# Kernel tuning notes

Measured on AMD Instinct MI355X. Metric: run time of the kernel, lower is better.

The kernel has to match this reference:

```python
import jax, jax.numpy as jnp
import numpy as np
from jax import lax

WIN_H, WIN_W = 4, 7            # window_size
GRID_OFF = (0.0, 40.0)         # grid_offsets
SPATIAL_SCALE = 1.0 / 0.4      # 1 / featmap_stride
BN_EPS = 1e-3


def setup_inputs() -> dict:
    key = jax.random.key(0)
    ks = jax.random.split(key, 4)
    B, Cin, H, W, N, P = 4, 256, 200, 176, 2048, 28
    x = jax.random.normal(ks[0], (B, Cin, H, W), jnp.float32)
    # realistic KITTI-style 3D boxes: x,y,z,w,l,h,r
    u = jax.random.uniform(ks[1], (B, N, 7), jnp.float32)
    lo = jnp.array([0.0, -40.0, -3.0, 1.4, 3.2, 1.4, -np.pi], jnp.float32)
    hi = jnp.array([70.4, 40.0, 1.0, 2.0, 4.6, 1.8, np.pi], jnp.float32)
    boxes = lo + u * (hi - lo)
    conv1_w = jax.random.normal(ks[2], (P, Cin, 3, 3), jnp.float32) * 0.02
    conv2_w = jax.random.normal(ks[3], (P, P, 1, 1), jnp.float32) * 0.1
    bn_gamma = jnp.ones((P,), jnp.float32)
    bn_beta = jnp.zeros((P,), jnp.float32)
    bn_mean = jnp.zeros((P,), jnp.float32)
    bn_var = jnp.ones((P,), jnp.float32)
    return dict(x=x, boxes=boxes, conv1_w=conv1_w, bn_gamma=bn_gamma,
                bn_beta=bn_beta, bn_mean=bn_mean, bn_var=bn_var, conv2_w=conv2_w)


def _bilinear_zeros(img, xs, ys):
    # img: (H, W); xs, ys: (N,) pixel coords. Zeros padding, align_corners=True
    # semantics (the torch code normalizes by (W-1)/(H-1), i.e. pixel coords).
    H, W = img.shape
    x0 = jnp.floor(xs)
    y0 = jnp.floor(ys)
    x1 = x0 + 1.0
    y1 = y0 + 1.0

    def gather(yi, xi):
        valid = (xi >= 0) & (xi <= W - 1) & (yi >= 0) & (yi <= H - 1)
        xi_c = jnp.clip(xi, 0, W - 1).astype(jnp.int32)
        yi_c = jnp.clip(yi, 0, H - 1).astype(jnp.int32)
        return jnp.where(valid, img[yi_c, xi_c], 0.0)

    Ia = gather(y0, x0)
    Ib = gather(y1, x0)
    Ic = gather(y0, x1)
    Id = gather(y1, x1)
    wa = (x1 - xs) * (y1 - ys)
    wb = (x1 - xs) * (ys - y0)
    wc = (xs - x0) * (y1 - ys)
    wd = (xs - x0) * (ys - y0)
    return wa * Ia + wb * Ib + wc * Ic + wd * Id


def reference(x, boxes, conv1_w, bn_gamma, bn_beta, bn_mean, bn_var, conv2_w):
    dn = ('NCHW', 'OIHW', 'NCHW')
    feat = lax.conv_general_dilated(x, conv1_w, (1, 1), 'SAME', dimension_numbers=dn)
    inv_std = bn_gamma / jnp.sqrt(bn_var + BN_EPS)
    scale = inv_std[None, :, None, None]
    shift = (bn_beta - bn_mean * inv_std)[None, :, None, None]
    feat = jax.nn.relu(feat * scale + shift)
    feat = lax.conv_general_dilated(feat, conv2_w, (1, 1), 'SAME', dimension_numbers=dn)  # (B,P,H,W)

    # rotated sampling grid: boxes[:, :, [0,1,3,4,6]] = (x, y, w, l, r)
    xg, yg, wg, lg, rg = (boxes[..., i] for i in (0, 1, 3, 4, 6))  # each (B,N)
    cosT = jnp.cos(rg)[..., None, None]
    sinT = jnp.sin(rg)[..., None, None]
    lin_x = jnp.linspace(-0.5, 0.5, WIN_H)[:, None]     # (4,1)
    lin_y = jnp.linspace(-0.5, 0.5, WIN_W)[None, :]     # (1,7)
    xx = lin_x * wg[..., None, None]                    # (B,N,4,1)
    yy = lin_y * lg[..., None, None]                    # (B,N,1,7)
    gx = xx * cosT + yy * sinT + xg[..., None, None]    # (B,N,4,7)
    gy = yy * cosT - xx * sinT + yg[..., None, None]    # (B,N,4,7)
    gx = (gx + GRID_OFF[0]) * SPATIAL_SCALE
    gy = (gy + GRID_OFF[1]) * SPATIAL_SCALE
    B, N = xg.shape
    P = WIN_H * WIN_W
    gx = gx.transpose(0, 2, 3, 1).reshape(B, P, N)      # (B,28,N), part = window cell
    gy = gy.transpose(0, 2, 3, 1).reshape(B, P, N)

    # each part-channel p samples its own window cell -> (B,P,N)
    sample = jax.vmap(jax.vmap(_bilinear_zeros))
    out = sample(feat, gx, gy)                          # (B,P,N)
    scores = out.mean(axis=1)                           # (B,N) mean over parts
    return scores.reshape(-1)                           # torch.cat over batch
```

## Files before the change

### kernel.cpp

```cpp
#include <hip/hip_runtime.h>
#include <hip/hip_bf16.h>


#define WDIM 176
#define HDIM 200
#define HWDIM 35200
#define CIN 256
#define PDIM 28
#define NBOX 2048

typedef __attribute__((ext_vector_type(8))) short bf16x8;
typedef __attribute__((ext_vector_type(4))) float floatx4;
typedef __attribute__((ext_vector_type(16))) float floatx16;

__device__ __forceinline__ unsigned short f2bf(float f) {
    unsigned int u; __builtin_memcpy(&u, &f, 4);
    unsigned int r = u + 0x7FFFu + ((u >> 16) & 1u);
    return (unsigned short)(r >> 16);
}

__global__ __launch_bounds__(256) void transpose_kernel(const float* __restrict__ x,
                                                        unsigned short* __restrict__ xT2) {
    __shared__ unsigned short st[64][72];
    int b = blockIdx.z, c0 = blockIdx.y * 64, px0 = blockIdx.x * 64;
    int t = threadIdx.x;

    int c_l = t >> 2, pq = t & 3;
    const float* sp = x + (long)(b * CIN + c0 + c_l) * HWDIM + px0 + pq * 16;
    float4 v0 = ((const float4*)sp)[0], v1 = ((const float4*)sp)[1];
    float4 v2 = ((const float4*)sp)[2], v3 = ((const float4*)sp)[3];
    int pr = pq * 16;
    st[pr +  0][c_l] = f2bf(v0.x); st[pr +  1][c_l] = f2bf(v0.y);
    st[pr +  2][c_l] = f2bf(v0.z); st[pr +  3][c_l] = f2bf(v0.w);
    st[pr +  4][c_l] = f2bf(v1.x); st[pr +  5][c_l] = f2bf(v1.y);
    st[pr +  6][c_l] = f2bf(v1.z); st[pr +  7][c_l] = f2bf(v1.w);
    st[pr +  8][c_l] = f2bf(v2.x); st[pr +  9][c_l] = f2bf(v2.y);
    st[pr + 10][c_l] = f2bf(v2.z); st[pr + 11][c_l] = f2bf(v2.w);
    st[pr + 12][c_l] = f2bf(v3.x); st[pr + 13][c_l] = f2bf(v3.y);
    st[pr + 14][c_l] = f2bf(v3.z); st[pr + 15][c_l] = f2bf(v3.w);
    __syncthreads();

    int w = t >> 6, l = t & 63;
    int ks = (c0 >> 4) + w;
    long pbase = ((long)(b * 16 + ks) * HWDIM + px0) * 16;
#pragma unroll
    for (int i = 0; i < 2; i++) {
        int px_l = i * 32 + (l >> 1);
        int hc = l & 1;
        bf16x8 frag = *(const bf16x8*)&st[px_l][w * 16 + hc * 8];
        *(bf16x8*)(xT2 + pbase + px_l * 16 + hc * 8) = frag;
    }
}

__global__ void prep_kernel(const float* __restrict__ w1,
                            const float* __restrict__ g, const float* __restrict__ bt,
                            const float* __restrict__ mn, const float* __restrict__ vr,
                            unsigned short* __restrict__ BwT2,
                            float* __restrict__ scale, float* __restrict__ shift) {
    int idx = blockIdx.x * 256 + threadIdx.x;
    if (idx < 9 * 16 * 64 * 8) {
        int f = idx >> 9;
        int tap = f >> 4, ks = f & 15;
        int l = (idx >> 3) & 63;
        int e = idx & 7;
        int n = l & 31, kh = l >> 5;
        int c = ks * 16 + kh * 8 + e;
        BwT2[idx] = (n < PDIM) ? f2bf(w1[n * 2304 + c * 9 + tap]) : (unsigned short)0;
    } else if (idx < 73728 + 32) {
        int p = idx - 73728;
        if (p < PDIM) {
            float inv = g[p] / sqrtf(vr[p] + 1e-3f);
            scale[p] = inv;
            shift[p] = bt[p] - mn[p] * inv;
        } else { scale[p] = 0.f; shift[p] = 0.f; }
    }
}

__global__ __launch_bounds__(64) void conv1_kernel(const unsigned short* __restrict__ xT2,
                                                   const unsigned short* __restrict__ BwT2,
                                                   const float* __restrict__ scale,
                                                   const float* __restrict__ shift,
                                                   const float* __restrict__ w2,
                                                   float* __restrict__ feat2) {
    __shared__ float t2f[32 * 36];

    int wg = blockIdx.y * 1200 + blockIdx.x;
    int nl = (wg & 7) * 600 + (wg >> 3);
    int b = nl / 1200;
    int rem = nl - b * 1200;
    int y = rem / 6, win = rem - (rem / 6) * 6;
    int pxbase = win * 32;

    int lane = threadIdx.x;
    int r32 = lane & 31, khalf = lane >> 5;

    bool rowok[3];
#pragma unroll
    for (int rr = 0; rr < 3; rr++) rowok[rr] = (y + rr - 1 >= 0) && (y + rr - 1 < HDIM);
    bool edge = (win == 0) || (win == 5);

    bool xval[3];
    int  voff[3];
#pragma unroll
    for (int d = 0; d < 3; d++) {
        int xp = pxbase + r32 + d - 1;
        xval[d] = (xp >= 0) && (xp < WDIM);
        int xc = xp < 0 ? 0 : (xp > WDIM - 1 ? WDIM - 1 : xp);
        voff[d] = xc * 32 + khalf * 16;
    }

    const char* abase[3];
#pragma unroll
    for (int rr = 0; rr < 3; rr++) {
        int yc = y + rr - 1;
        yc = yc < 0 ? 0 : (yc > HDIM - 1 ? HDIM - 1 : yc);
        abase[rr] = (const char*)xT2 + ((long)b * 16 * HWDIM + (long)yc * WDIM) * 32;
    }
    const long KS = (long)HWDIM * 32;
    const char* bb = (const char*)BwT2 + lane * 16;

    bf16x8 aq[2][9];
#pragma unroll
    for (int t = 0; t < 9; t++)
        aq[0][t] = *(const bf16x8*)(abase[t / 3] + voff[t % 3]);

    floatx16 acc = {};

#pragma unroll
    for (int s = 0; s < 16; s++) {
        const int cur = s & 1, nxt = cur ^ 1;
        bf16x8 bq[9];
#pragma unroll
        for (int t = 0; t < 9; t++)
            bq[t] = *(const bf16x8*)(bb + t * 16384 + s * 1024);
        if (s < 15) {
#pragma unroll
            for (int t = 0; t < 9; t++)
                aq[nxt][t] = *(const bf16x8*)(abase[t / 3] + KS * (s + 1) + voff[t % 3]);
            __builtin_amdgcn_sched_barrier(0);
            asm volatile("s_waitcnt vmcnt(18)" ::: "memory");
        } else {
            __builtin_amdgcn_sched_barrier(0);
            asm volatile("s_waitcnt vmcnt(9)" ::: "memory");
        }
        __builtin_amdgcn_sched_barrier(0);
        if (!edge) {
#pragma unroll
            for (int t = 0; t < 9; t++) {
                if (!rowok[t / 3]) continue;
                acc = __builtin_amdgcn_mfma_f32_32x32x16_bf16(aq[cur][t], bq[t], acc, 0, 0, 0);
            }
        } else {
#pragma unroll
            for (int t = 0; t < 9; t++) {
                if (!rowok[t / 3]) continue;
                bf16x8 af = aq[cur][t];
                if (!xval[t % 3]) af = (bf16x8)0;
                acc = __builtin_amdgcn_mfma_f32_32x32x16_bf16(af, bq[t], acc, 0, 0, 0);
            }
        }
    }

    {
        float sc = scale[r32], sh2 = shift[r32];
#pragma unroll
        for (int i = 0; i < 16; i++) {
            int prow = (i & 3) + 8 * (i >> 2) + 4 * khalf;
            float v = fmaf(acc[i], sc, sh2);
            t2f[prow * 36 + r32] = v > 0.f ? v : 0.f;
        }
    }
    long rowpix = (long)b * HWDIM + (long)y * WDIM;
    int n_l = r32;
    float4 w2r[7];
#pragma unroll
    for (int jj = 0; jj < 7; jj++) {
        if (n_l < PDIM) w2r[jj] = ((const float4*)(w2 + n_l * PDIM))[jj];
        else            w2r[jj] = make_float4(0.f, 0.f, 0.f, 0.f);
    }
#pragma unroll
    for (int i = 0; i < 16; i++) {
        int pxl = khalf * 16 + i;
        float s = 0.f;
#pragma unroll
        for (int jj = 0; jj < 7; jj++) {
            float4 a = *(const float4*)&t2f[pxl * 36 + jj * 4];
            s = fmaf(a.x, w2r[jj].x, s); s = fmaf(a.y, w2r[jj].y, s);
            s = fmaf(a.z, w2r[jj].z, s); s = fmaf(a.w, w2r[jj].w, s);
        }
        int px = pxbase + pxl;
        if (n_l < PDIM && px < WDIM) feat2[(rowpix + px) * PDIM + n_l] = s;
    }
}

__global__ __launch_bounds__(256) void sample_kernel(const float* __restrict__ boxes,
                                                     const float* __restrict__ feat2,
                                                     float* __restrict__ out) {
    int gid = blockIdx.x * 256 + threadIdx.x;
    int box = gid >> 5;
    int pl = gid & 31;
    int b = box >> 11;
    float val = 0.f;
    if (pl < PDIM) {
        long bb = (long)box * 7;
        float xg = boxes[bb + 0], yg = boxes[bb + 1];
        float wg = boxes[bb + 3], lg = boxes[bb + 4];
        float rg = boxes[bb + 6];
        float ct = cosf(rg), st = sinf(rg);
        const float lxv[4] = {-0.5f, -0.16666667f, 0.16666667f, 0.5f};
        const float lyv[7] = {-0.5f, -0.33333334f, -0.16666667f, 0.f,
                               0.16666667f, 0.33333334f, 0.5f};
        int h = pl / 7, ww = pl - (pl / 7) * 7;
        float xx = lxv[h] * wg;
        float yy = lyv[ww] * lg;
        float gx = (xx * ct + yy * st + xg) * 2.5f;
        float gy = (yy * ct - xx * st + yg + 40.f) * 2.5f;
        float x0 = floorf(gx), y0 = floorf(gy);
        float fx = gx - x0, fy = gy - y0;
        int xi = (int)x0, yi = (int)y0;
        const float* base = feat2 + (long)b * HWDIM * PDIM + pl;
        float Ia = 0.f, Ib = 0.f, Ic = 0.f, Id = 0.f;
        if (yi >= 0 && yi < HDIM) {
            long r0 = (long)yi * WDIM;
            if (xi >= 0 && xi < WDIM)         Ia = base[(r0 + xi) * PDIM];
            if (xi + 1 >= 0 && xi + 1 < WDIM) Ic = base[(r0 + xi + 1) * PDIM];
        }
        if (yi + 1 >= 0 && yi + 1 < HDIM) {
            long r1 = (long)(yi + 1) * WDIM;
            if (xi >= 0 && xi < WDIM)         Ib = base[(r1 + xi) * PDIM];
            if (xi + 1 >= 0 && xi + 1 < WDIM) Id = base[(r1 + xi + 1) * PDIM];
        }
        val = (1.f - fx) * (1.f - fy) * Ia + (1.f - fx) * fy * Ib
            + fx * (1.f - fy) * Ic + fx * fy * Id;
    }
#pragma unroll
    for (int m = 16; m >= 1; m >>= 1) val += __shfl_xor(val, m, 64);
    if ((threadIdx.x & 31) == 0) {
        out[box] = val * (1.f / 28.f);
    }
}

extern "C" void kernel_launch(void* const* d_in, const int* in_sizes, int n_in,
                              void* d_out, int out_size, void* d_ws, size_t ws_size,
                              hipStream_t stream) {
    const float* x     = (const float*)d_in[0];
    const float* boxes = (const float*)d_in[1];
    const float* w1    = (const float*)d_in[2];
    const float* g     = (const float*)d_in[3];
    const float* bt    = (const float*)d_in[4];
    const float* mn    = (const float*)d_in[5];
    const float* vr    = (const float*)d_in[6];
    const float* w2    = (const float*)d_in[7];
    float* out = (float*)d_out;

    char* ws = (char*)d_ws;
    unsigned short* xT2  = (unsigned short*)ws;
    float* feat2         = (float*)(ws + 72089600);
    unsigned short* BwT2 = (unsigned short*)(ws + 90112000);
    float* scale         = (float*)(ws + 90259456);
    float* shift         = (float*)(ws + 90259584);

    transpose_kernel<<<dim3(550, 4, 4), 256, 0, stream>>>(x, xT2);
    prep_kernel<<<289, 256, 0, stream>>>(w1, g, bt, mn, vr, BwT2, scale, shift);
    conv1_kernel<<<dim3(1200, 4), 64, 0, stream>>>(xT2, BwT2, scale, shift, w2, feat2);
    sample_kernel<<<1024, 256, 0, stream>>>(boxes, feat2, out);
}
```

Baseline: 284.9 us.

## Share conv weight tiles across six waves via async global-to-LDS staging

The conv1 kernel changes from one 64-thread wave per 32-pixel window to a 384-thread block covering a whole image row with six waves. The weight (B) fragments are no longer loaded by every wave from global memory. The block loads them once with global_load_lds async copies into a 6-slot LDS ring and reads them from LDS, using manual vmcnt waits and barriers to pipeline this. The aim is to cut redundant weight traffic from global memory, at the cost of block-level barriers, more LDS use and tighter manual wait counting.

```diff
diff --git a/kernel.cpp b/kernel.cpp
--- a/kernel.cpp
+++ b/kernel.cpp
@@ -17,6 +17,12 @@
     unsigned int u; __builtin_memcpy(&u, &f, 4);
     unsigned int r = u + 0x7FFFu + ((u >> 16) & 1u);
     return (unsigned short)(r >> 16);
+}
+
+__device__ __forceinline__ void async_copy16(const void* g, void* l) {
+    __builtin_amdgcn_global_load_lds(
+        (const __attribute__((address_space(1))) void*)g,
+        (__attribute__((address_space(3))) void*)l, 16, 0, 0);
 }
 
 __global__ __launch_bounds__(256) void transpose_kernel(const float* __restrict__ x,
@@ -76,28 +82,27 @@
     }
 }
 
-__global__ __launch_bounds__(64) void conv1_kernel(const unsigned short* __restrict__ xT2,
-                                                   const unsigned short* __restrict__ BwT2,
-                                                   const float* __restrict__ scale,
-                                                   const float* __restrict__ shift,
-                                                   const float* __restrict__ w2,
-                                                   float* __restrict__ feat2) {
-    __shared__ float t2f[32 * 36];
-
-    int wg = blockIdx.y * 1200 + blockIdx.x;
-    int nl = (wg & 7) * 600 + (wg >> 3);
-    int b = nl / 1200;
-    int rem = nl - b * 1200;
-    int y = rem / 6, win = rem - (rem / 6) * 6;
-    int pxbase = win * 32;
-
-    int lane = threadIdx.x;
+__global__ __launch_bounds__(384) void conv1_kernel(const unsigned short* __restrict__ xT2,
+                                                    const unsigned short* __restrict__ BwT2,
+                                                    const float* __restrict__ scale,
+                                                    const float* __restrict__ shift,
+                                                    const float* __restrict__ w2,
+                                                    float* __restrict__ feat2) {
+    __shared__ unsigned short Bs[6 * 9 * 512];
+
+    int wg = blockIdx.y * 200 + blockIdx.x;
+    int nl = (wg & 7) * 100 + (wg >> 3);
+    int b = nl / 200, y = nl % 200;
+
+    int lane = threadIdx.x & 63, w = threadIdx.x >> 6;
     int r32 = lane & 31, khalf = lane >> 5;
+    int lane16 = lane * 16;
+    int pxbase = w * 32;
 
     bool rowok[3];
 #pragma unroll
     for (int rr = 0; rr < 3; rr++) rowok[rr] = (y + rr - 1 >= 0) && (y + rr - 1 < HDIM);
-    bool edge = (win == 0) || (win == 5);
+    bool edge = (w == 0) || (w == 5);
 
     bool xval[3];
     int  voff[3];
@@ -117,50 +122,91 @@
         abase[rr] = (const char*)xT2 + ((long)b * 16 * HWDIM + (long)yc * WDIM) * 32;
     }
     const long KS = (long)HWDIM * 32;
-    const char* bb = (const char*)BwT2 + lane * 16;
-
+    const char* bwb = (const char*)BwT2;
+
+#define STAGE_PAIR(s2) {                                                      \
+        _Pragma("unroll")                                                     \
+        for (int k = 0; k < 3; k++) {                                         \
+            int F = 3 * w + k;                                                \
+            int stp = (s2) + (F >= 9 ? 1 : 0);                                \
+            int tap = F >= 9 ? F - 9 : F;                                     \
+            async_copy16(bwb + tap * 16384 + stp * 1024 + lane16,             \
+                         (char*)Bs + (stp % 6) * 9216 + tap * 1024);          \
+        }                                                                     \
+    }
+
+    STAGE_PAIR(0)
+    STAGE_PAIR(2)
     bf16x8 aq[2][9];
 #pragma unroll
     for (int t = 0; t < 9; t++)
         aq[0][t] = *(const bf16x8*)(abase[t / 3] + voff[t % 3]);
+    __builtin_amdgcn_sched_barrier(0);
+    asm volatile("s_waitcnt vmcnt(9)" ::: "memory");
+    __builtin_amdgcn_sched_barrier(0);
+    asm volatile("s_barrier" ::: "memory");
 
     floatx16 acc = {};
 
-#pragma unroll
-    for (int s = 0; s < 16; s++) {
-        const int cur = s & 1, nxt = cur ^ 1;
-        bf16x8 bq[9];
-#pragma unroll
-        for (int t = 0; t < 9; t++)
-            bq[t] = *(const bf16x8*)(bb + t * 16384 + s * 1024);
-        if (s < 15) {
+#define DO_MFMA(AQ)                                                           \
+        if (!edge) {                                                          \
+            _Pragma("unroll")                                                 \
+            for (int t = 0; t < 9; t++) {                                     \
+                if (!rowok[t / 3]) continue;                                  \
+                acc = __builtin_amdgcn_mfma_f32_32x32x16_bf16(AQ[t], bq[t], acc, 0, 0, 0); \
+            }                                                                 \
+        } else {                                                              \
+            _Pragma("unroll")                                                 \
+            for (int t = 0; t < 9; t++) {                                     \
+                if (!rowok[t / 3]) continue;                                  \
+                bf16x8 af = AQ[t];                                            \
+                if (!xval[t % 3]) af = (bf16x8)0;                             \
+                acc = __builtin_amdgcn_mfma_f32_32x32x16_bf16(af, bq[t], acc, 0, 0, 0); \
+            }                                                                 \
+        }
+
+#pragma unroll
+    for (int S = 0; S < 8; S++) {
+        const int s0 = 2 * S, s1 = 2 * S + 1;
+        {
+            if (S <= 5) STAGE_PAIR(2 * S + 4)
 #pragma unroll
             for (int t = 0; t < 9; t++)
-                aq[nxt][t] = *(const bf16x8*)(abase[t / 3] + KS * (s + 1) + voff[t % 3]);
+                aq[1][t] = *(const bf16x8*)(abase[t / 3] + KS * s1 + voff[t % 3]);
+            bf16x8 bq[9];
+#pragma unroll
+            for (int t = 0; t < 9; t++)
+                bq[t] = *(const bf16x8*)((const char*)Bs + (s0 % 6) * 9216 + t * 1024 + lane16);
             __builtin_amdgcn_sched_barrier(0);
-            asm volatile("s_waitcnt vmcnt(18)" ::: "memory");
-        } else {
+            if (S <= 5) { asm volatile("s_waitcnt vmcnt(12)" ::: "memory"); }
+            else        { asm volatile("s_waitcnt vmcnt(9)"  ::: "memory"); }
             __builtin_amdgcn_sched_barrier(0);
-            asm volatile("s_waitcnt vmcnt(9)" ::: "memory");
-        }
-        __builtin_amdgcn_sched_barrier(0);
-        if (!edge) {
-#pragma unroll
-            for (int t = 0; t < 9; t++) {
-                if (!rowok[t / 3]) continue;
-                acc = __builtin_amdgcn_mfma_f32_32x32x16_bf16(aq[cur][t], bq[t], acc, 0, 0, 0);
+            DO_MFMA(aq[0])
+        }
+        {
+            if (S <= 6) {
+#pragma unroll
+                for (int t = 0; t < 9; t++)
+                    aq[0][t] = *(const bf16x8*)(abase[t / 3] + KS * (s1 + 1) + voff[t % 3]);
             }
-        } else {
-#pragma unroll
-            for (int t = 0; t < 9; t++) {
-                if (!rowok[t / 3]) continue;
-                bf16x8 af = aq[cur][t];
-                if (!xval[t % 3]) af = (bf16x8)0;
-                acc = __builtin_amdgcn_mfma_f32_32x32x16_bf16(af, bq[t], acc, 0, 0, 0);
-            }
-        }
-    }
-
+            bf16x8 bq[9];
+#pragma unroll
+            for (int t = 0; t < 9; t++)
+                bq[t] = *(const bf16x8*)((const char*)Bs + (s1 % 6) * 9216 + t * 1024 + lane16);
+            __builtin_amdgcn_sched_barrier(0);
+            if (S <= 6) { asm volatile("s_waitcnt vmcnt(9)" ::: "memory"); }
+            else        { asm volatile("s_waitcnt vmcnt(0)" ::: "memory"); }
+            __builtin_amdgcn_sched_barrier(0);
+            DO_MFMA(aq[1])
+            if (S <= 5) { asm volatile("s_barrier" ::: "memory"); }
+        }
+    }
+#undef DO_MFMA
+#undef STAGE_PAIR
+
+    __syncthreads();
+
+    float* t2f = (float*)Bs + w * (32 * 36);
     {
         float sc = scale[r32], sh2 = shift[r32];
 #pragma unroll
@@ -262,6 +308,6 @@
 
     transpose_kernel<<<dim3(550, 4, 4), 256, 0, stream>>>(x, xT2);
     prep_kernel<<<289, 256, 0, stream>>>(w1, g, bt, mn, vr, BwT2, scale, shift);
-    conv1_kernel<<<dim3(1200, 4), 64, 0, stream>>>(xT2, BwT2, scale, shift, w2, feat2);
+    conv1_kernel<<<dim3(200, 4), 384, 0, stream>>>(xT2, BwT2, scale, shift, w2, feat2);
     sample_kernel<<<1024, 256, 0, stream>>>(boxes, feat2, out);
 }
```

Result: slower. 301.6 us (+5.9%).

## Compute two 32-pixel MFMA tiles per conv workgroup to reuse weight fragments

Applied to the files above, without the earlier changes.

Each conv1 workgroup now covers 64 pixels of a row, as two 32-pixel M tiles with separate accumulators, instead of 32 pixels. The grid is halved to match. Each loaded weight fragment feeds two MFMA tiles, which halves weight loads per output pixel. Activation prefetch for the second tile is interleaved after the first tile's MFMAs, and the wait counts are adjusted to match. The cost is more VGPRs for the doubled activation buffers and fewer workgroups, which can lower occupancy and latency hiding.

```diff
diff --git a/kernel.cpp b/kernel.cpp
--- a/kernel.cpp
+++ b/kernel.cpp
@@ -84,12 +84,12 @@
                                                    float* __restrict__ feat2) {
     __shared__ float t2f[32 * 36];
 
-    int wg = blockIdx.y * 1200 + blockIdx.x;
-    int nl = (wg & 7) * 600 + (wg >> 3);
-    int b = nl / 1200;
-    int rem = nl - b * 1200;
-    int y = rem / 6, win = rem - (rem / 6) * 6;
-    int pxbase = win * 32;
+    int wg = blockIdx.y * 600 + blockIdx.x;
+    int nl = (wg & 7) * 300 + (wg >> 3);
+    int b = nl / 600;
+    int rem = nl - b * 600;
+    int y = rem / 3, win = rem - (rem / 3) * 3;
+    int pxbase = win * 64;
 
     int lane = threadIdx.x;
     int r32 = lane & 31, khalf = lane >> 5;
@@ -97,16 +97,19 @@
     bool rowok[3];
 #pragma unroll
     for (int rr = 0; rr < 3; rr++) rowok[rr] = (y + rr - 1 >= 0) && (y + rr - 1 < HDIM);
-    bool edge = (win == 0) || (win == 5);
-
-    bool xval[3];
-    int  voff[3];
-#pragma unroll
-    for (int d = 0; d < 3; d++) {
-        int xp = pxbase + r32 + d - 1;
-        xval[d] = (xp >= 0) && (xp < WDIM);
-        int xc = xp < 0 ? 0 : (xp > WDIM - 1 ? WDIM - 1 : xp);
-        voff[d] = xc * 32 + khalf * 16;
+    bool edge0 = (win == 0), edge1 = (win == 2);
+
+    bool xval[2][3];
+    int  voff[2][3];
+#pragma unroll
+    for (int mt = 0; mt < 2; mt++) {
+#pragma unroll
+        for (int d = 0; d < 3; d++) {
+            int xp = pxbase + mt * 32 + r32 + d - 1;
+            xval[mt][d] = (xp >= 0) && (xp < WDIM);
+            int xc = xp < 0 ? 0 : (xp > WDIM - 1 ? WDIM - 1 : xp);
+            voff[mt][d] = xc * 32 + khalf * 16;
+        }
     }
 
     const char* abase[3];
@@ -119,12 +122,12 @@
     const long KS = (long)HWDIM * 32;
     const char* bb = (const char*)BwT2 + lane * 16;
 
-    bf16x8 aq[2][9];
-#pragma unroll
-    for (int t = 0; t < 9; t++)
-        aq[0][t] = *(const bf16x8*)(abase[t / 3] + voff[t % 3]);
-
-    floatx16 acc = {};
+    bf16x8 aq[2][18];
+#pragma unroll
+    for (int f = 0; f < 18; f++)
+        aq[0][f] = *(const bf16x8*)(abase[(f % 9) / 3] + voff[f / 9][f % 3]);
+
+    floatx16 acc0 = {}, acc1 = {};
 
 #pragma unroll
     for (int s = 0; s < 16; s++) {
@@ -136,60 +139,87 @@
         if (s < 15) {
 #pragma unroll
             for (int t = 0; t < 9; t++)
-                aq[nxt][t] = *(const bf16x8*)(abase[t / 3] + KS * (s + 1) + voff[t % 3]);
+                aq[nxt][t] = *(const bf16x8*)(abase[t / 3] + KS * (s + 1) + voff[0][t % 3]);
             __builtin_amdgcn_sched_barrier(0);
-            asm volatile("s_waitcnt vmcnt(18)" ::: "memory");
+            asm volatile("s_waitcnt vmcnt(9)" ::: "memory");
         } else {
             __builtin_amdgcn_sched_barrier(0);
-            asm volatile("s_waitcnt vmcnt(9)" ::: "memory");
+            asm volatile("s_waitcnt vmcnt(0)" ::: "memory");
         }
         __builtin_amdgcn_sched_barrier(0);
-        if (!edge) {
-#pragma unroll
-            for (int t = 0; t < 9; t++) {
-                if (!rowok[t / 3]) continue;
-                acc = __builtin_amdgcn_mfma_f32_32x32x16_bf16(aq[cur][t], bq[t], acc, 0, 0, 0);
+
+        if (!edge0) {
+#pragma unroll
+            for (int t = 0; t < 9; t++) {
+                if (!rowok[t / 3]) continue;
+                acc0 = __builtin_amdgcn_mfma_f32_32x32x16_bf16(aq[cur][t], bq[t], acc0, 0, 0, 0);
             }
         } else {
 #pragma unroll
             for (int t = 0; t < 9; t++) {
                 if (!rowok[t / 3]) continue;
                 bf16x8 af = aq[cur][t];
-                if (!xval[t % 3]) af = (bf16x8)0;
-                acc = __builtin_amdgcn_mfma_f32_32x32x16_bf16(af, bq[t], acc, 0, 0, 0);
-            }
-        }
-    }
-
-    {
-        float sc = scale[r32], sh2 = shift[r32];
+                if (!xval[0][t % 3]) af = (bf16x8)0;
+                acc0 = __builtin_amdgcn_mfma_f32_32x32x16_bf16(af, bq[t], acc0, 0, 0, 0);
+            }
+        }
+
+        if (s < 15) {
+#pragma unroll
+            for (int t = 0; t < 9; t++)
+                aq[nxt][9 + t] = *(const bf16x8*)(abase[t / 3] + KS * (s + 1) + voff[1][t % 3]);
+        }
+        __builtin_amdgcn_sched_barrier(0);
+
+        if (!edge1) {
+#pragma unroll
+            for (int t = 0; t < 9; t++) {
+                if (!rowok[t / 3]) continue;
+                acc1 = __builtin_amdgcn_mfma_f32_32x32x16_bf16(aq[cur][9 + t], bq[t], acc1, 0, 0, 0);
+            }
+        } else {
+#pragma unroll
+            for (int t = 0; t < 9; t++) {
+                if (!rowok[t / 3]) continue;
+                bf16x8 af = aq[cur][9 + t];
+                if (!xval[1][t % 3]) af = (bf16x8)0;
+                acc1 = __builtin_amdgcn_mfma_f32_32x32x16_bf16(af, bq[t], acc1, 0, 0, 0);
+            }
+        }
+    }
+
+    long rowpix = (long)b * HWDIM + (long)y * WDIM;
+    int n_l = r32;
+    float4 w2r[7];
+#pragma unroll
+    for (int jj = 0; jj < 7; jj++) {
+        if (n_l < PDIM) w2r[jj] = ((const float4*)(w2 + n_l * PDIM))[jj];
+        else            w2r[jj] = make_float4(0.f, 0.f, 0.f, 0.f);
+    }
+    float sc = scale[r32], sh2 = shift[r32];
+
+#pragma unroll
+    for (int mt = 0; mt < 2; mt++) {
+        const floatx16& acc = mt ? acc1 : acc0;
 #pragma unroll
         for (int i = 0; i < 16; i++) {
             int prow = (i & 3) + 8 * (i >> 2) + 4 * khalf;
             float v = fmaf(acc[i], sc, sh2);
             t2f[prow * 36 + r32] = v > 0.f ? v : 0.f;
         }
-    }
-    long rowpix = (long)b * HWDIM + (long)y * WDIM;
-    int n_l = r32;
-    float4 w2r[7];
-#pragma unroll
-    for (int jj = 0; jj < 7; jj++) {
-        if (n_l < PDIM) w2r[jj] = ((const float4*)(w2 + n_l * PDIM))[jj];
-        else            w2r[jj] = make_float4(0.f, 0.f, 0.f, 0.f);
-    }
-#pragma unroll
-    for (int i = 0; i < 16; i++) {
-        int pxl = khalf * 16 + i;
-        float s = 0.f;
-#pragma unroll
-        for (int jj = 0; jj < 7; jj++) {
-            float4 a = *(const float4*)&t2f[pxl * 36 + jj * 4];
-            s = fmaf(a.x, w2r[jj].x, s); s = fmaf(a.y, w2r[jj].y, s);
-            s = fmaf(a.z, w2r[jj].z, s); s = fmaf(a.w, w2r[jj].w, s);
-        }
-        int px = pxbase + pxl;
-        if (n_l < PDIM && px < WDIM) feat2[(rowpix + px) * PDIM + n_l] = s;
+#pragma unroll
+        for (int i = 0; i < 16; i++) {
+            int pxl = khalf * 16 + i;
+            float s = 0.f;
+#pragma unroll
+            for (int jj = 0; jj < 7; jj++) {
+                float4 a = *(const float4*)&t2f[pxl * 36 + jj * 4];
+                s = fmaf(a.x, w2r[jj].x, s); s = fmaf(a.y, w2r[jj].y, s);
+                s = fmaf(a.z, w2r[jj].z, s); s = fmaf(a.w, w2r[jj].w, s);
+            }
+            int px = pxbase + mt * 32 + pxl;
+            if (n_l < PDIM && px < WDIM) feat2[(rowpix + px) * PDIM + n_l] = s;
+        }
     }
 }
 
@@ -262,6 +292,6 @@
 
     transpose_kernel<<<dim3(550, 4, 4), 256, 0, stream>>>(x, xT2);
     prep_kernel<<<289, 256, 0, stream>>>(w1, g, bt, mn, vr, BwT2, scale, shift);
-    conv1_kernel<<<dim3(1200, 4), 64, 0, stream>>>(xT2, BwT2, scale, shift, w2, feat2);
+    conv1_kernel<<<dim3(600, 4), 64, 0, stream>>>(xT2, BwT2, scale, shift, w2, feat2);
     sample_kernel<<<1024, 256, 0, stream>>>(boxes, feat2, out);
 }
```

New measurement: 286.4 us. No clear change (+0.5%).
